# Kernel optimization log

Measured on AMD Instinct MI355X. Metric: run time of the kernel, lower is better.

The kernel has to match this reference:

```python
import jax, jax.numpy as jnp
import numpy as np

NODES = 23   # 22 players + ball per frame-graph
K = 8        # random neighbors per node
B, T = 64, 128
G = B * T            # total graphs (frames)
N = G * NODES        # total nodes
D_IN, H, RH = 16, 128, 128


def setup_inputs() -> dict:
    key = jax.random.key(0)
    ks = jax.random.split(key, 10)
    x = jax.random.normal(ks[0], (N, D_IN), jnp.float32)
    # per-graph random edges: dst = each node repeated K times, src = random node in same graph
    src_local = jax.random.randint(ks[1], (G, NODES * K), 0, NODES)
    dst_local = jnp.tile(jnp.repeat(jnp.arange(NODES), K)[None, :], (G, 1))
    off = (jnp.arange(G) * NODES)[:, None]
    edge_index = jnp.stack([(src_local + off).reshape(-1),
                            (dst_local + off).reshape(-1)]).astype(jnp.int32)
    runner_idx = jax.random.randint(ks[2], (G,), 0, NODES, dtype=jnp.int32)
    sc = lambda k, sh: (jax.random.normal(k, sh, jnp.float32) * 0.05)
    return {
        'x': x, 'edge_index': edge_index, 'runner_idx': runner_idx,
        'W1': sc(ks[3], (D_IN, H)), 'b1': jnp.zeros((H,), jnp.float32),
        'W2': sc(ks[4], (H, H)),    'b2': jnp.zeros((H,), jnp.float32),
        'W_ih': sc(ks[5], (3 * RH, H)), 'W_hh': sc(ks[6], (3 * RH, RH)),
        'b_ih': jnp.zeros((3 * RH,), jnp.float32), 'b_hh': jnp.zeros((3 * RH,), jnp.float32),
        'Wp': sc(ks[7], (RH, 2)), 'bp': jnp.zeros((2,), jnp.float32),
    }


def _gcn_conv(h, edge_index, W, b):
    # PyG GCNConv: add self-loops, symmetric normalization, scatter-sum
    h = h @ W
    loop = jnp.arange(N, dtype=edge_index.dtype)
    s = jnp.concatenate([edge_index[0], loop])
    d = jnp.concatenate([edge_index[1], loop])
    deg = jax.ops.segment_sum(jnp.ones_like(s, h.dtype), d, num_segments=N)
    dinv = jnp.where(deg > 0, jax.lax.rsqrt(deg), 0.0)
    norm = dinv[s] * dinv[d]                      # [E+N]
    out = jax.ops.segment_sum(h[s] * norm[:, None], d, num_segments=N)
    return out + b


def _gru(seq, W_ih, W_hh, b_ih, b_hh):
    # torch GRU: gates in r,z,n order
    xg = seq @ W_ih.T + b_ih                      # [B,T,3RH]
    def step(hprev, xt):
        gh = hprev @ W_hh.T + b_hh
        xr, xz, xn = jnp.split(xt, 3, axis=-1)
        hr, hz, hn = jnp.split(gh, 3, axis=-1)
        r = jax.nn.sigmoid(xr + hr)
        z = jax.nn.sigmoid(xz + hz)
        n = jnp.tanh(xn + r * hn)
        hnew = (1.0 - z) * n + z * hprev
        return hnew, hnew
    h0 = jnp.zeros((seq.shape[0], RH), seq.dtype)
    _, outs = jax.lax.scan(step, h0, jnp.swapaxes(xg, 0, 1))
    return jnp.swapaxes(outs, 0, 1)               # [B,T,RH]


def reference(x, edge_index, runner_idx, W1, b1, W2, b2,
              W_ih, W_hh, b_ih, b_hh, Wp, bp):
    h = jax.nn.relu(_gcn_conv(x, edge_index, W1, b1))
    h = jax.nn.relu(_gcn_conv(h, edge_index, W2, b2))
    # fused equivalent of the per-graph nonzero()/indexing loop:
    runner_global = jnp.arange(G, dtype=jnp.int32) * NODES + runner_idx
    seq = h[runner_global].reshape(B, T, H)       # all lengths == T, padding is a no-op
    out = _gru(seq, W_ih, W_hh, b_ih, b_hh)
    return out @ Wp + bp                          # [B,T,2]
```

## Files before the change

kernel.cpp:

```cpp
#include <hip/hip_runtime.h>
#include <hip/hip_bf16.h>
#include <math.h>

#define GG 8192
#define NODESN 23
#define KK 8
#define DIN 16
#define HH 128
#define RHH 128
#define EPG (NODESN*KK)
#define TTT 128
#define BBB 64

template<int CTRL>
static __device__ __forceinline__ float dpp_add(float v) {
    int x = __builtin_amdgcn_update_dpp(0, __float_as_int(v), CTRL, 0xF, 0xF, true);
    return v + __int_as_float(x);
}
#define DPP_XOR1 0xB1
#define DPP_XOR2 0x4E
#define DPP_MIR7 0x141
#define DPP_SHL4 0x104

__global__ __launch_bounds__(256) void gcn_hsum(
    const float* __restrict__ x, const int* __restrict__ esrc,
    const int* __restrict__ runner,
    const float* __restrict__ W1, const float* __restrict__ b1,
    float* __restrict__ hsum_g)
{
    __shared__ float xs[NODESN * DIN];
    __shared__ int   srcs[EPG];
    __shared__ float t1[NODESN * HH];
    __shared__ float red[256];

    const int g   = blockIdx.x;
    const int tid = threadIdx.x;
    const int j   = tid & 127;
    const int nh  = tid >> 7;

    for (int i = tid; i < NODESN * DIN; i += 256) xs[i] = x[g * NODESN * DIN + i];
    for (int i = tid; i < EPG; i += 256)          srcs[i] = esrc[g * EPG + i] - g * NODESN;

    float w[DIN];
    #pragma unroll
    for (int k = 0; k < DIN; k++) w[k] = W1[k * HH + j];
    const float b1j = b1[j];
    __syncthreads();

    const int n0 = nh * 12;
    const int n1 = nh ? NODESN : 12;
    for (int n = n0; n < n1; n++) {
        float acc = 0.f;
        #pragma unroll
        for (int k = 0; k < DIN; k += 4) {
            float4 xv = *(const float4*)&xs[n * DIN + k];
            acc = fmaf(xv.x, w[k], fmaf(xv.y, w[k+1], fmaf(xv.z, w[k+2], fmaf(xv.w, w[k+3], acc))));
        }
        t1[n * HH + j] = acc;
    }
    __syncthreads();

    const int r = runner[g];
    float part = 0.f;
    for (int slot = nh; slot < 9; slot += 2) {
        int node = (slot < 8) ? srcs[r * KK + slot] : r;
        float acc = t1[node * HH + j];
        #pragma unroll
        for (int k = 0; k < KK; k++) acc += t1[srcs[node * KK + k] * HH + j];
        part += fmaxf(acc * (1.f / 9.f) + b1j, 0.f);
    }
    red[tid] = part;
    __syncthreads();
    if (tid < HH) hsum_g[(size_t)g * HH + tid] = red[tid] + red[tid + 128];
}

__global__ __launch_bounds__(256) void seq_kernel(
    const float* __restrict__ hsum_g, const float* __restrict__ W2,
    const float* __restrict__ b2, float* __restrict__ seq)
{
    __shared__ float hs[16 * HH];
    const int tid = threadIdx.x;
    const int j = tid & 127, mh = tid >> 7;
    const size_t base = (size_t)blockIdx.x * 16 * HH;

    for (int v = tid; v < 16 * HH / 4; v += 256)
        ((float4*)hs)[v] = ((const float4*)(hsum_g + base))[v];
    __syncthreads();

    float acc[8];
    #pragma unroll
    for (int m = 0; m < 8; m++) acc[m] = 0.f;
    const float* hrow = hs + mh * 8 * HH;
    for (int k = 0; k < HH; k += 4) {
        float w0  = W2[(k+0)*HH + j];
        float w1  = W2[(k+1)*HH + j];
        float w2v = W2[(k+2)*HH + j];
        float w3  = W2[(k+3)*HH + j];
        #pragma unroll
        for (int m = 0; m < 8; m++) {
            float4 hv = *(const float4*)&hrow[m * HH + k];
            acc[m] = fmaf(hv.x, w0, fmaf(hv.y, w1, fmaf(hv.z, w2v, fmaf(hv.w, w3, acc[m]))));
        }
    }
    const float bj = b2[j];
    #pragma unroll
    for (int m = 0; m < 8; m++)
        seq[base + (size_t)(mh * 8 + m) * HH + j] = fmaxf(acc[m] * (1.f/9.f) + bj, 0.f);
}

__global__ void transpose_wih(const float* __restrict__ W, float* __restrict__ WT)
{
    int idx = blockIdx.x * 256 + threadIdx.x;
    if (idx < 3 * RHH * RHH) {
        int jj = idx / RHH, kk = idx - jj * RHH;
        WT[kk * (3 * RHH) + jj] = W[idx];
    }
}

__global__ __launch_bounds__(384) void xg_kernel(
    const float* __restrict__ seq, const float* __restrict__ WT,
    const float* __restrict__ b_ih, float* __restrict__ xg)
{
    const int tid = threadIdx.x;
    const int m0 = blockIdx.x * 8;
    const float* srow = seq + (size_t)m0 * RHH;
    float acc[8];
    const float bv = b_ih[tid];
    #pragma unroll
    for (int mi = 0; mi < 8; mi++) acc[mi] = bv;
    for (int k = 0; k < RHH; k += 4) {
        float w0 = WT[(k+0)*384 + tid];
        float w1 = WT[(k+1)*384 + tid];
        float w2 = WT[(k+2)*384 + tid];
        float w3 = WT[(k+3)*384 + tid];
        #pragma unroll
        for (int mi = 0; mi < 8; mi++) {
            float4 sv = *(const float4*)(srow + mi * RHH + k);
            acc[mi] = fmaf(sv.x, w0, fmaf(sv.y, w1, fmaf(sv.z, w2, fmaf(sv.w, w3, acc[mi]))));
        }
    }
    #pragma unroll
    for (int mi = 0; mi < 8; mi++)
        xg[(size_t)(m0 + mi) * 384 + tid] = acc[mi];
}

#define CHUNK 32
#define XGB_FLOATS (CHUNK * HH * 4)

__global__ __launch_bounds__(512)
__attribute__((amdgpu_waves_per_eu(2, 2)))
void gru_kernel(
    const float* __restrict__ xg, const float* __restrict__ W_hh,
    const float* __restrict__ b_hh, const float* __restrict__ Wp,
    const float* __restrict__ bp, float* __restrict__ out)
{
    __shared__ float xgbuf[XGB_FLOATS];
    __shared__ float houtb[(CHUNK + 2) * HH];
    __shared__ float wps[2 * RHH + 2];

    const int b   = blockIdx.x;
    const int tid = threadIdx.x;
    const int kq  = tid & 7;
    const int i0  = tid >> 3;
    const int uhf = kq >> 2;
    const int u   = 2 * i0 + uhf;

    float4 wr0[4], wz0[4], wn0[4], wr1[4], wz1[4], wn1[4];
    int hof[4];
    {
        const float* w0 = W_hh + (size_t)(2 * i0) * RHH + kq * 16;
        #pragma unroll
        for (int m = 0; m < 4; m++) {
            const int off = 4 * ((m + kq) & 3);
            hof[m] = kq * 16 + off;
            wr0[m] = *(const float4*)(w0 + off);
            wz0[m] = *(const float4*)(w0 + RHH * RHH + off);
            wn0[m] = *(const float4*)(w0 + 2 * RHH * RHH + off);
            wr1[m] = *(const float4*)(w0 + RHH + off);
            wz1[m] = *(const float4*)(w0 + RHH * RHH + RHH + off);
            wn1[m] = *(const float4*)(w0 + 2 * RHH * RHH + RHH + off);
        }
    }
    const float bhr = b_hh[u];
    const float bhz = b_hh[RHH + u];
    const float bhn = b_hh[2 * RHH + u];

    if (tid < 2 * RHH) wps[tid] = Wp[tid];
    if (tid < 2)       wps[2 * RHH + tid] = bp[tid];
    if (tid < HH)      houtb[CHUNK * HH + tid] = 0.f;
    float hprev = 0.f;

    const float* xbase = xg + (size_t)b * TTT * 3 * RHH;
    float* outb = out + (size_t)b * TTT * 2;

    for (int c = 0; c < TTT / CHUNK; c++) {
        #pragma unroll
        for (int k2 = 0; k2 < 8; k2++) {
            int slot = tid + (k2 << 9);
            int tl = slot >> 7, ii = slot & 127;
            const float* gsrc = xbase + (size_t)(c * CHUNK + tl) * 384 + ii;
            float4 v;
            v.x = gsrc[0]; v.y = gsrc[128]; v.z = gsrc[256]; v.w = 0.f;
            *(float4*)&xgbuf[slot << 2] = v;
        }
        if (c > 0) {
            const int s  = tid & 7;
            const int cc = (tid >> 3) & 1;
            const int tl = tid >> 4;
            const float* hr = &houtb[(tl + 1) * HH + s * 16];
            float acc = 0.f;
            #pragma unroll
            for (int m = 0; m < 16; m += 4) {
                float4 hv = *(const float4*)(hr + m);
                int k = s * 16 + m;
                acc = fmaf(hv.x, wps[(k+0)*2 + cc],
                      fmaf(hv.y, wps[(k+1)*2 + cc],
                      fmaf(hv.z, wps[(k+2)*2 + cc],
                      fmaf(hv.w, wps[(k+3)*2 + cc], acc))));
            }
            acc = dpp_add<DPP_XOR1>(acc);
            acc = dpp_add<DPP_XOR2>(acc);
            acc = dpp_add<DPP_SHL4>(acc);
            if (s == 0)
                outb[((c - 1) * CHUNK + tl) * 2 + cc] = acc + wps[2 * RHH + cc];
        }
        __syncthreads();

        float4 xgv = *(const float4*)&xgbuf[u << 2];
        for (int tl = 0; tl < CHUNK; tl++) {
            const float* hrow = &houtb[(tl == 0 ? CHUNK : tl) * HH];
            float4 xgn = xgv;
            if (tl + 1 < CHUNK)
                xgn = *(const float4*)&xgbuf[((tl + 1) * HH + u) << 2];

            float ar0 = 0.f, az0 = 0.f, an0 = 0.f;
            float ar1 = 0.f, az1 = 0.f, an1 = 0.f;
            #pragma unroll
            for (int m = 0; m < 4; m++) {
                float4 hv = *(const float4*)(hrow + hof[m]);
                ar0 = fmaf(hv.x, wr0[m].x, fmaf(hv.y, wr0[m].y, fmaf(hv.z, wr0[m].z, fmaf(hv.w, wr0[m].w, ar0))));
                az0 = fmaf(hv.x, wz0[m].x, fmaf(hv.y, wz0[m].y, fmaf(hv.z, wz0[m].z, fmaf(hv.w, wz0[m].w, az0))));
                an0 = fmaf(hv.x, wn0[m].x, fmaf(hv.y, wn0[m].y, fmaf(hv.z, wn0[m].z, fmaf(hv.w, wn0[m].w, an0))));
                ar1 = fmaf(hv.x, wr1[m].x, fmaf(hv.y, wr1[m].y, fmaf(hv.z, wr1[m].z, fmaf(hv.w, wr1[m].w, ar1))));
                az1 = fmaf(hv.x, wz1[m].x, fmaf(hv.y, wz1[m].y, fmaf(hv.z, wz1[m].z, fmaf(hv.w, wz1[m].w, az1))));
                an1 = fmaf(hv.x, wn1[m].x, fmaf(hv.y, wn1[m].y, fmaf(hv.z, wn1[m].z, fmaf(hv.w, wn1[m].w, an1))));
            }
            ar0 = dpp_add<DPP_XOR1>(ar0); ar0 = dpp_add<DPP_XOR2>(ar0); ar0 = dpp_add<DPP_MIR7>(ar0);
            az0 = dpp_add<DPP_XOR1>(az0); az0 = dpp_add<DPP_XOR2>(az0); az0 = dpp_add<DPP_MIR7>(az0);
            an0 = dpp_add<DPP_XOR1>(an0); an0 = dpp_add<DPP_XOR2>(an0); an0 = dpp_add<DPP_MIR7>(an0);
            ar1 = dpp_add<DPP_XOR1>(ar1); ar1 = dpp_add<DPP_XOR2>(ar1); ar1 = dpp_add<DPP_MIR7>(ar1);
            az1 = dpp_add<DPP_XOR1>(az1); az1 = dpp_add<DPP_XOR2>(az1); az1 = dpp_add<DPP_MIR7>(az1);
            an1 = dpp_add<DPP_XOR1>(an1); an1 = dpp_add<DPP_XOR2>(an1); an1 = dpp_add<DPP_MIR7>(an1);

            float ar = uhf ? ar1 : ar0;
            float az = uhf ? az1 : az0;
            float an = uhf ? an1 : an0;

            float sr = xgv.x + ar + bhr;
            float sz = xgv.y + az + bhz;
            float rg = 1.f / (1.f + __expf(-sr));
            float zg = 1.f / (1.f + __expf(-sz));
            float tv = fmaf(rg, an + bhn, xgv.z);
            tv = fminf(fmaxf(tv, -15.f), 15.f);
            float e2 = __expf(-2.f * tv);
            float ng = (1.f - e2) / (1.f + e2);
            hprev = fmaf(zg, hprev, (1.f - zg) * ng);
            if ((kq & 3) == 0) houtb[(tl + 1) * HH + u] = hprev;
            xgv = xgn;
            __syncthreads();
        }
    }

    {
        const int s  = tid & 7;
        const int cc = (tid >> 3) & 1;
        const int tl = tid >> 4;
        const float* hr = &houtb[(tl + 1) * HH + s * 16];
        float acc = 0.f;
        #pragma unroll
        for (int m = 0; m < 16; m += 4) {
            float4 hv = *(const float4*)(hr + m);
            int k = s * 16 + m;
            acc = fmaf(hv.x, wps[(k+0)*2 + cc],
                  fmaf(hv.y, wps[(k+1)*2 + cc],
                  fmaf(hv.z, wps[(k+2)*2 + cc],
                  fmaf(hv.w, wps[(k+3)*2 + cc], acc))));
        }
        acc = dpp_add<DPP_XOR1>(acc);
        acc = dpp_add<DPP_XOR2>(acc);
        acc = dpp_add<DPP_SHL4>(acc);
        if (s == 0)
            outb[((TTT / CHUNK - 1) * CHUNK + tl) * 2 + cc] = acc + wps[2 * RHH + cc];
    }
}

extern "C" void kernel_launch(void* const* d_in, const int* in_sizes, int n_in,
                              void* d_out, int out_size, void* d_ws, size_t ws_size,
                              hipStream_t stream)
{
    const float* x      = (const float*)d_in[0];
    const int*   eidx   = (const int*)d_in[1];
    const int*   runner = (const int*)d_in[2];
    const float* W1     = (const float*)d_in[3];
    const float* b1     = (const float*)d_in[4];
    const float* W2     = (const float*)d_in[5];
    const float* b2     = (const float*)d_in[6];
    const float* W_ih   = (const float*)d_in[7];
    const float* W_hh   = (const float*)d_in[8];
    const float* b_ih   = (const float*)d_in[9];
    const float* b_hh   = (const float*)d_in[10];
    const float* Wp     = (const float*)d_in[11];
    const float* bp     = (const float*)d_in[12];
    float* out = (float*)d_out;

    float* seq    = (float*)d_ws;
    float* xg     = seq + (size_t)GG * HH;
    float* WT     = xg + (size_t)GG * 3 * RHH;
    float* hsum_g = xg;

    transpose_wih<<<192, 256, 0, stream>>>(W_ih, WT);
    gcn_hsum<<<GG, 256, 0, stream>>>(x, eidx, runner, W1, b1, hsum_g);
    seq_kernel<<<GG / 16, 256, 0, stream>>>(hsum_g, W2, b2, seq);
    xg_kernel<<<GG / 8, 384, 0, stream>>>(seq, WT, b_ih, xg);
    gru_kernel<<<BBB, 512, 0, stream>>>(xg, W_hh, b_hh, Wp, bp, out);
}
```

Before: 245.7 us.

## Fuse GCN aggregation and W2 projection into one kernel processing four graphs per block

```diff
diff --git a/kernel.cpp b/kernel.cpp
--- a/kernel.cpp
+++ b/kernel.cpp
@@ -22,90 +22,91 @@
 #define DPP_MIR7 0x141
 #define DPP_SHL4 0x104
 
-__global__ __launch_bounds__(256) void gcn_hsum(
+__global__ __launch_bounds__(256) void gcn_fused(
     const float* __restrict__ x, const int* __restrict__ esrc,
     const int* __restrict__ runner,
     const float* __restrict__ W1, const float* __restrict__ b1,
-    float* __restrict__ hsum_g)
-{
-    __shared__ float xs[NODESN * DIN];
-    __shared__ int   srcs[EPG];
-    __shared__ float t1[NODESN * HH];
-    __shared__ float red[256];
-
-    const int g   = blockIdx.x;
-    const int tid = threadIdx.x;
-    const int j   = tid & 127;
-    const int nh  = tid >> 7;
-
-    for (int i = tid; i < NODESN * DIN; i += 256) xs[i] = x[g * NODESN * DIN + i];
-    for (int i = tid; i < EPG; i += 256)          srcs[i] = esrc[g * EPG + i] - g * NODESN;
+    const float* __restrict__ W2, const float* __restrict__ b2,
+    float* __restrict__ seq)
+{
+    __shared__ float t1[4 * NODESN * HH];
+    __shared__ int   srcs[4 * EPG];
+    __shared__ float red4[4 * 256];
+    __shared__ float hs[4 * HH];
+
+    const int g0   = blockIdx.x * 4;
+    const int tid  = threadIdx.x;
+    const int j    = tid & 127;
+    const int half = tid >> 7;
+
+    for (int i = tid; i < 4 * EPG; i += 256) {
+        int gg = i / EPG;
+        srcs[i] = esrc[(size_t)g0 * EPG + i] - (g0 + gg) * NODESN;
+    }
 
     float w[DIN];
     #pragma unroll
     for (int k = 0; k < DIN; k++) w[k] = W1[k * HH + j];
     const float b1j = b1[j];
+
+    const int n0 = half ? 12 : 0;
+    const int n1 = half ? NODESN : 12;
+    for (int gg = 0; gg < 4; gg++) {
+        const float* xgp = x + (size_t)(g0 + gg) * NODESN * DIN;
+        for (int n = n0; n < n1; n++) {
+            const float4* xr = (const float4*)(xgp + n * DIN);
+            float4 a0 = xr[0], a1 = xr[1], a2 = xr[2], a3 = xr[3];
+            float acc;
+            acc = fmaf(a0.x, w[0],  fmaf(a0.y, w[1],  fmaf(a0.z, w[2],  fmaf(a0.w, w[3],
+                  fmaf(a1.x, w[4],  fmaf(a1.y, w[5],  fmaf(a1.z, w[6],  fmaf(a1.w, w[7],
+                  fmaf(a2.x, w[8],  fmaf(a2.y, w[9],  fmaf(a2.z, w[10], fmaf(a2.w, w[11],
+                  fmaf(a3.x, w[12], fmaf(a3.y, w[13], fmaf(a3.z, w[14], fmaf(a3.w, w[15],
+                  0.f))))))))))))))));
+            t1[((gg * NODESN + n) << 7) + j] = acc;
+        }
+    }
     __syncthreads();
 
-    const int n0 = nh * 12;
-    const int n1 = nh ? NODESN : 12;
-    for (int n = n0; n < n1; n++) {
-        float acc = 0.f;
-        #pragma unroll
-        for (int k = 0; k < DIN; k += 4) {
-            float4 xv = *(const float4*)&xs[n * DIN + k];
-            acc = fmaf(xv.x, w[k], fmaf(xv.y, w[k+1], fmaf(xv.z, w[k+2], fmaf(xv.w, w[k+3], acc))));
-        }
-        t1[n * HH + j] = acc;
+    for (int gg = 0; gg < 4; gg++) {
+        const int r = runner[g0 + gg];
+        const int* sg = srcs + gg * EPG;
+        const float* tg = t1 + ((gg * NODESN) << 7);
+        float part = 0.f;
+        for (int slot = half; slot < 9; slot += 2) {
+            int node = (slot < 8) ? sg[r * KK + slot] : r;
+            float acc = tg[(node << 7) + j];
+            #pragma unroll
+            for (int k = 0; k < KK; k++) acc += tg[(sg[node * KK + k] << 7) + j];
+            part += fmaxf(acc * (1.f / 9.f) + b1j, 0.f);
+        }
+        red4[gg * 256 + tid] = part;
     }
     __syncthreads();
 
-    const int r = runner[g];
-    float part = 0.f;
-    for (int slot = nh; slot < 9; slot += 2) {
-        int node = (slot < 8) ? srcs[r * KK + slot] : r;
-        float acc = t1[node * HH + j];
-        #pragma unroll
-        for (int k = 0; k < KK; k++) acc += t1[srcs[node * KK + k] * HH + j];
-        part += fmaxf(acc * (1.f / 9.f) + b1j, 0.f);
-    }
-    red[tid] = part;
+    {
+        int gg = tid >> 7, jj = tid & 127;
+        hs[gg * HH + jj]       = red4[gg * 256 + jj]       + red4[gg * 256 + jj + 128];
+        hs[(gg + 2) * HH + jj] = red4[(gg + 2) * 256 + jj] + red4[(gg + 2) * 256 + jj + 128];
+    }
     __syncthreads();
-    if (tid < HH) hsum_g[(size_t)g * HH + tid] = red[tid] + red[tid + 128];
-}
-
-__global__ __launch_bounds__(256) void seq_kernel(
-    const float* __restrict__ hsum_g, const float* __restrict__ W2,
-    const float* __restrict__ b2, float* __restrict__ seq)
-{
-    __shared__ float hs[16 * HH];
-    const int tid = threadIdx.x;
-    const int j = tid & 127, mh = tid >> 7;
-    const size_t base = (size_t)blockIdx.x * 16 * HH;
-
-    for (int v = tid; v < 16 * HH / 4; v += 256)
-        ((float4*)hs)[v] = ((const float4*)(hsum_g + base))[v];
-    __syncthreads();
-
-    float acc[8];
-    #pragma unroll
-    for (int m = 0; m < 8; m++) acc[m] = 0.f;
-    const float* hrow = hs + mh * 8 * HH;
-    for (int k = 0; k < HH; k += 4) {
-        float w0  = W2[(k+0)*HH + j];
-        float w1  = W2[(k+1)*HH + j];
-        float w2v = W2[(k+2)*HH + j];
-        float w3  = W2[(k+3)*HH + j];
-        #pragma unroll
-        for (int m = 0; m < 8; m++) {
-            float4 hv = *(const float4*)&hrow[m * HH + k];
-            acc[m] = fmaf(hv.x, w0, fmaf(hv.y, w1, fmaf(hv.z, w2v, fmaf(hv.w, w3, acc[m]))));
-        }
-    }
-    const float bj = b2[j];
-    #pragma unroll
-    for (int m = 0; m < 8; m++)
-        seq[base + (size_t)(mh * 8 + m) * HH + j] = fmaxf(acc[m] * (1.f/9.f) + bj, 0.f);
+
+    {
+        const float b2j = b2[j];
+        const float* h0 = hs + (half * 2) * HH;
+        float acc0 = 0.f, acc1 = 0.f;
+        for (int k = 0; k < HH; k += 4) {
+            float w0  = W2[(k + 0) * HH + j];
+            float w1  = W2[(k + 1) * HH + j];
+            float w2v = W2[(k + 2) * HH + j];
+            float w3  = W2[(k + 3) * HH + j];
+            float4 hv0 = *(const float4*)(h0 + k);
+            float4 hv1 = *(const float4*)(h0 + HH + k);
+            acc0 = fmaf(hv0.x, w0, fmaf(hv0.y, w1, fmaf(hv0.z, w2v, fmaf(hv0.w, w3, acc0))));
+            acc1 = fmaf(hv1.x, w0, fmaf(hv1.y, w1, fmaf(hv1.z, w2v, fmaf(hv1.w, w3, acc1))));
+        }
+        seq[(size_t)(g0 + half * 2 + 0) * HH + j] = fmaxf(acc0 * (1.f / 9.f) + b2j, 0.f);
+        seq[(size_t)(g0 + half * 2 + 1) * HH + j] = fmaxf(acc1 * (1.f / 9.f) + b2j, 0.f);
+    }
 }
 
 __global__ void transpose_wih(const float* __restrict__ W, float* __restrict__ WT)
@@ -313,14 +314,12 @@
     const float* bp     = (const float*)d_in[12];
     float* out = (float*)d_out;
 
-    float* seq    = (float*)d_ws;
-    float* xg     = seq + (size_t)GG * HH;
-    float* WT     = xg + (size_t)GG * 3 * RHH;
-    float* hsum_g = xg;
+    float* seq = (float*)d_ws;
+    float* xg  = seq + (size_t)GG * HH;
+    float* WT  = xg + (size_t)GG * 3 * RHH;
 
     transpose_wih<<<192, 256, 0, stream>>>(W_ih, WT);
-    gcn_hsum<<<GG, 256, 0, stream>>>(x, eidx, runner, W1, b1, hsum_g);
-    seq_kernel<<<GG / 16, 256, 0, stream>>>(hsum_g, W2, b2, seq);
+    gcn_fused<<<GG / 4, 256, 0, stream>>>(x, eidx, runner, W1, b1, W2, b2, seq);
     xg_kernel<<<GG / 8, 384, 0, stream>>>(seq, WT, b_ih, xg);
     gru_kernel<<<BBB, 512, 0, stream>>>(xg, W_hh, b_hh, Wp, bp, out);
 }
```

After: 289.5 us. 17.8% more time.
